# Optimization experiments

Hardware: AMD Instinct MI355X
Metric: run time of the kernel (lower is better)

Reference implementation:

```python
import jax, jax.numpy as jnp
import numpy as np

C = 256
C8 = C // 8  # query/key channels
B, T, W, H = 4, 8, 32, 32


def setup_inputs() -> dict:
    key = jax.random.key(0)
    ks = jax.random.split(key, 8)
    s = 0.05
    return {
        "x": jax.random.normal(ks[0], (B, C, T, W, H), dtype=jnp.float32),
        "wq": jax.random.normal(ks[1], (C8, C), dtype=jnp.float32) * s,
        "bq": jax.random.normal(ks[2], (C8,), dtype=jnp.float32) * s,
        "wk": jax.random.normal(ks[3], (C8, C), dtype=jnp.float32) * s,
        "bk": jax.random.normal(ks[4], (C8,), dtype=jnp.float32) * s,
        "wv": jax.random.normal(ks[5], (C, C), dtype=jnp.float32) * s,
        "bv": jax.random.normal(ks[6], (C,), dtype=jnp.float32) * s,
        "gamma": jax.random.normal(ks[7], (1,), dtype=jnp.float32),
    }


def reference(x, wq, bq, wk, bk, wv, bv, gamma):
    b, c, t, w, h = x.shape
    n = w * h
    # Faithful to torch: x.view(-1, c, w, h) is a row-major reinterpretation
    xr = jnp.reshape(x, (-1, c, n))  # (m, C, N), m = B*T
    # 1x1 convs == per-pixel linear projections
    q = jnp.einsum("oc,mcn->mno", wq, xr) + bq            # (m, N, C8)
    k = jnp.einsum("oc,mcn->mon", wk, xr) + bk[:, None]   # (m, C8, N)
    v = jnp.einsum("oc,mcn->mon", wv, xr) + bv[:, None]   # (m, C, N)
    energy = jnp.einsum("mic,mcj->mij", q, k)             # (m, N, N), unscaled
    attention = jax.nn.softmax(energy, axis=-1)
    out = jnp.einsum("mcn,mnj->mcj", v, attention)        # V @ A (as in torch code)
    out = jnp.reshape(out, (b, c, t, w, h))
    return gamma * out + x
```

## Files before the change

### kernel.cpp

```cpp
#include <hip/hip_runtime.h>

#define MB    32
#define CCH   256
#define QCH   32
#define NPIX  1024
#define SLICE (CCH * NPIX)
#define L2E   1.44269504088896340736f
#define SHIFT 32.0f

typedef __bf16          bf16x8 __attribute__((ext_vector_type(8)));
typedef __bf16          bf16x4 __attribute__((ext_vector_type(4)));
typedef float           f32x4  __attribute__((ext_vector_type(4)));
typedef unsigned int    u32x4  __attribute__((ext_vector_type(4)));
typedef unsigned short  u16x4  __attribute__((ext_vector_type(4)));

__device__ __forceinline__ unsigned short f2bf(float f) {
    unsigned int u = __builtin_bit_cast(unsigned int, f);
    u += 0x7FFFu + ((u >> 16) & 1u);
    return (unsigned short)(u >> 16);
}
__device__ __forceinline__ u16x4 cvt4(float a, float b, float c, float d) {
    bf16x4 v = { (__bf16)a, (__bf16)b, (__bf16)c, (__bf16)d };
    return __builtin_bit_cast(u16x4, v);
}
__device__ __forceinline__ float bf2f(unsigned short u) {
    unsigned int v = (unsigned int)u << 16;
    return __builtin_bit_cast(float, v);
}
__device__ __forceinline__ bf16x8 ldfrag(const unsigned short* p) {
    u32x4 u = *(const u32x4*)p;
    return __builtin_bit_cast(bf16x8, u);
}

#define WB_OFF  0u
#define QT_OFF  262144u
#define KT_OFF  2359296u
#define V_OFF   4456448u
#define A2F_OFF 21233664u

__global__ __launch_bounds__(256) void k_prep_w(
    const float* __restrict__ wq, const float* __restrict__ wk,
    const float* __restrict__ wv, unsigned short* __restrict__ Wb)
{
    int i4 = (blockIdx.x * 256 + threadIdx.x) * 4;
    int o = i4 >> 8, c = i4 & 255;
    const float* src = (o < 32) ? wq + (size_t)o * CCH + c
                     : (o < 64) ? wk + (size_t)(o - 32) * CCH + c
                                : wv + (size_t)(o - 64) * CCH + c;
    float4 v = *(const float4*)src;
    *(u16x4*)(Wb + i4) = cvt4(v.x, v.y, v.z, v.w);
}

__global__ __launch_bounds__(256) void k_proj(
    const float* __restrict__ x, const unsigned short* __restrict__ Wb,
    const float* __restrict__ bq, const float* __restrict__ bk,
    const float* __restrict__ bv,
    unsigned short* __restrict__ Qt, unsigned short* __restrict__ Kt,
    unsigned short* __restrict__ V)
{
    __shared__ unsigned short Xs[64 * 268];

    const int t = threadIdx.x, lane = t & 63, w = t >> 6;
    const int lj = lane & 15, q = lane >> 4;
    const int n0 = blockIdx.x * 64;
    const int mi = blockIdx.y;
    const float* xp = x + (size_t)mi * SLICE;

#pragma unroll
    for (int r = 0; r < 8; ++r) {
        int job = t + r * 256;
        int cp = job >> 4;
        int seg = job & 15;
        float4 va = *(const float4*)(xp + (size_t)(2 * cp) * NPIX + n0 + seg * 4);
        float4 vb = *(const float4*)(xp + (size_t)(2 * cp + 1) * NPIX + n0 + seg * 4);
        u16x4 da = cvt4(va.x, va.y, va.z, va.w);
        u16x4 db = cvt4(vb.x, vb.y, vb.z, vb.w);
#pragma unroll
        for (int e = 0; e < 4; ++e) {
            unsigned pk = (unsigned)da[e] | ((unsigned)db[e] << 16);
            *(unsigned*)&Xs[(seg * 4 + e) * 268 + 2 * cp] = pk;
        }
    }
    __syncthreads();

    f32x4 acc[5][4];
#pragma unroll
    for (int i = 0; i < 5; ++i)
#pragma unroll
        for (int b = 0; b < 4; ++b) acc[i][b] = (f32x4){0.f, 0.f, 0.f, 0.f};

    const unsigned short* wbase = Wb + (size_t)(w * 16 + lj) * CCH + q * 8;
    const unsigned short* xbase = &Xs[lj * 268 + q * 8];

#pragma unroll 2
    for (int kc = 0; kc < CCH; kc += 32) {
        bf16x8 a[5];
#pragma unroll
        for (int i = 0; i < 5; ++i)
            a[i] = ldfrag(wbase + (size_t)i * 64 * CCH + kc);
        bf16x8 xb[4];
#pragma unroll
        for (int b = 0; b < 4; ++b)
            xb[b] = ldfrag(xbase + b * 16 * 268 + kc);
#pragma unroll
        for (int i = 0; i < 5; ++i)
#pragma unroll
            for (int b = 0; b < 4; ++b)
                acc[i][b] = (i == 0)
                    ? __builtin_amdgcn_mfma_f32_16x16x32_bf16(a[i], xb[b], acc[i][b], 0, 0, 0)
                    : __builtin_amdgcn_mfma_f32_16x16x32_bf16(xb[b], a[i], acc[i][b], 0, 0, 0);
    }

#pragma unroll
    for (int i = 0; i < 5; ++i) {
        if (i == 0) {
            const int ob = w * 16 + 4 * q;
            if (w < 2) {
                unsigned short* Qp = Qt + (size_t)mi * NPIX * QCH;
                float b0 = bq[ob], b1 = bq[ob + 1], b2 = bq[ob + 2], b3 = bq[ob + 3];
#pragma unroll
                for (int b = 0; b < 4; ++b) {
                    int n = n0 + b * 16 + lj;
                    *(u16x4*)(Qp + (size_t)n * QCH + ob) =
                        cvt4((acc[i][b][0] + b0) * L2E, (acc[i][b][1] + b1) * L2E,
                             (acc[i][b][2] + b2) * L2E, (acc[i][b][3] + b3) * L2E);
                }
            } else {
                unsigned short* Kp = Kt + (size_t)mi * NPIX * QCH;
                int o2 = ob - 32;
                float b0 = bk[o2], b1 = bk[o2 + 1], b2 = bk[o2 + 2], b3 = bk[o2 + 3];
#pragma unroll
                for (int b = 0; b < 4; ++b) {
                    int n = n0 + b * 16 + lj;
                    *(u16x4*)(Kp + (size_t)n * QCH + o2) =
                        cvt4(acc[i][b][0] + b0, acc[i][b][1] + b1,
                             acc[i][b][2] + b2, acc[i][b][3] + b3);
                }
            }
        } else {
            unsigned short* Vw = V + (size_t)mi * SLICE;
            const int c16 = w + 4 * (i - 1);
            const float bb = bv[c16 * 16 + lj];
            const int n05 = n0 >> 5;
#pragma unroll
            for (int b = 0; b < 4; ++b) {
                const int l = lj | (((b & 1) * 2 + (q >> 1)) << 4);
                size_t base = ((size_t)(c16 * 32 + n05 + (b >> 1)) * 64 + l) * 8 + (q & 1) * 4;
                *(u16x4*)(Vw + base) = cvt4(acc[i][b][0] + bb, acc[i][b][1] + bb,
                                            acc[i][b][2] + bb, acc[i][b][3] + bb);
            }
        }
    }
}

__global__ __launch_bounds__(256) void k_stats(
    const unsigned short* __restrict__ Qt, const unsigned short* __restrict__ Kt,
    float* __restrict__ a2f)
{
    const int t = threadIdx.x, lane = t & 63, w = t >> 6;
    const int lj = lane & 15, q = lane >> 4;
    const int n16 = blockIdx.x * 64 + w * 16;
    const int mi = blockIdx.y;
    const unsigned short* Qp = Qt + (size_t)mi * NPIX * QCH;
    const unsigned short* Kp = Kt + (size_t)mi * NPIX * QCH;

    bf16x8 qa = ldfrag(Qp + (size_t)(n16 + lj) * QCH + q * 8);

    float s[4] = { 0.f, 0.f, 0.f, 0.f };
#pragma unroll 8
    for (int jc = 0; jc < NPIX; jc += 16) {
        bf16x8 kb = ldfrag(Kp + (size_t)(jc + lj) * QCH + q * 8);
        f32x4 z = (f32x4){0.f, 0.f, 0.f, 0.f};
        f32x4 e = __builtin_amdgcn_mfma_f32_16x16x32_bf16(qa, kb, z, 0, 0, 0);
#pragma unroll
        for (int r = 0; r < 4; ++r) s[r] += exp2f(e[r] - SHIFT);
    }
#pragma unroll
    for (int msk = 1; msk <= 8; msk <<= 1)
#pragma unroll
        for (int r = 0; r < 4; ++r) s[r] += __shfl_xor(s[r], msk, 64);
    if (lj == 0) {
        float* apo = a2f + (size_t)mi * NPIX;
#pragma unroll
        for (int r = 0; r < 4; ++r)
            apo[n16 + 4 * q + r] = SHIFT + log2f(s[r]);
    }
}

__global__ __launch_bounds__(256) void k_fused(
    const float* __restrict__ x, const float* __restrict__ gamma,
    const unsigned short* __restrict__ Qt, const unsigned short* __restrict__ Kt,
    const unsigned short* __restrict__ Vf, const float* __restrict__ a2f,
    float* __restrict__ out)
{
    __shared__ unsigned short Vs[2][8192];
    __shared__ unsigned short Ps[4][32][36];

    const int b = blockIdx.x;
    const int mi  = (b & 7) | ((b >> 7) << 3);
    const int sub = (b >> 3) & 15;
    const int j0  = (sub & 7) * 128;
    const int cb  = sub >> 3;

    const int t = threadIdx.x, lane = t & 63, w = t >> 6;
    const int lj = lane & 15, q = lane >> 4;
    const int jw = j0 + w * 32;

    const unsigned short* Qp = Qt + (size_t)mi * NPIX * QCH;
    const unsigned short* Kp = Kt + (size_t)mi * NPIX * QCH;
    const unsigned short* Vp = Vf + (size_t)mi * SLICE;
    const float* ap = a2f + (size_t)mi * NPIX;

    bf16x8 kb[2];
#pragma unroll
    for (int sj = 0; sj < 2; ++sj)
        kb[sj] = ldfrag(Kp + (size_t)(jw + sj * 16 + lj) * QCH + q * 8);

    const int fs = t >> 5, ln0 = (t & 31) * 2;
    const unsigned short* vsrc0 = Vp + ((size_t)(cb * 8 + fs) * 32) * 512 + ln0 * 8;

    f32x4 acc[8][2];
#pragma unroll
    for (int ci = 0; ci < 8; ++ci)
#pragma unroll
        for (int ji = 0; ji < 2; ++ji) acc[ci][ji] = (f32x4){0.f, 0.f, 0.f, 0.f};

    {
        u32x4 a0 = *(const u32x4*)(vsrc0);
        u32x4 a1 = *(const u32x4*)(vsrc0 + 8);
        u32x4 b0 = *(const u32x4*)(vsrc0 + 512);
        u32x4 b1 = *(const u32x4*)(vsrc0 + 520);
        *(u32x4*)&Vs[0][fs * 512 + ln0 * 8]            = a0;
        *(u32x4*)&Vs[0][fs * 512 + ln0 * 8 + 8]        = a1;
        *(u32x4*)&Vs[0][4096 + fs * 512 + ln0 * 8]     = b0;
        *(u32x4*)&Vs[0][4096 + fs * 512 + ln0 * 8 + 8] = b1;
    }
    bf16x8 qa[2][2];
    f32x4  a4[2][2];
#pragma unroll
    for (int h = 0; h < 2; ++h)
#pragma unroll
        for (int sn = 0; sn < 2; ++sn) {
            qa[h][sn] = ldfrag(Qp + (size_t)(h * 32 + sn * 16 + lj) * QCH + q * 8);
            a4[h][sn] = *(const f32x4*)(ap + h * 32 + sn * 16 + 4 * q);
        }
    __syncthreads();

    int p = 0;
    for (int nc = 0; nc < NPIX; nc += 64, p ^= 1) {
        const int n1 = (nc + 64) & (NPIX - 1);
        const unsigned short* vs = vsrc0 + (size_t)(n1 >> 5) * 512;
        u32x4 nv0 = *(const u32x4*)vs;
        u32x4 nv1 = *(const u32x4*)(vs + 8);
        u32x4 nv2 = *(const u32x4*)(vs + 512);
        u32x4 nv3 = *(const u32x4*)(vs + 520);
        bf16x8 qa_n[2][2];
        f32x4  a4_n[2][2];
#pragma unroll
        for (int h = 0; h < 2; ++h)
#pragma unroll
            for (int sn = 0; sn < 2; ++sn) {
                qa_n[h][sn] = ldfrag(Qp + (size_t)(n1 + h * 32 + sn * 16 + lj) * QCH + q * 8);
                a4_n[h][sn] = *(const f32x4*)(ap + n1 + h * 32 + sn * 16 + 4 * q);
            }

#pragma unroll
        for (int h = 0; h < 2; ++h) {
#pragma unroll
            for (int sj = 0; sj < 2; ++sj) {
                f32x4 z = (f32x4){0.f, 0.f, 0.f, 0.f};
                f32x4 e0 = __builtin_amdgcn_mfma_f32_16x16x32_bf16(qa[h][0], kb[sj], z, 0, 0, 0);
                f32x4 e1 = __builtin_amdgcn_mfma_f32_16x16x32_bf16(qa[h][1], kb[sj], z, 0, 0, 0);
                *(u16x4*)&Ps[w][sj * 16 + lj][4 * q] =
                    cvt4(exp2f(e0[0] - a4[h][0][0]), exp2f(e0[1] - a4[h][0][1]),
                         exp2f(e0[2] - a4[h][0][2]), exp2f(e0[3] - a4[h][0][3]));
                *(u16x4*)&Ps[w][sj * 16 + lj][16 + 4 * q] =
                    cvt4(exp2f(e1[0] - a4[h][1][0]), exp2f(e1[1] - a4[h][1][1]),
                         exp2f(e1[2] - a4[h][1][2]), exp2f(e1[3] - a4[h][1][3]));
            }
            bf16x8 pf[2];
#pragma unroll
            for (int ji = 0; ji < 2; ++ji)
                pf[ji] = ldfrag(&Ps[w][ji * 16 + lj][q * 8]);
            __builtin_amdgcn_s_setprio(1);
#pragma unroll
            for (int ci = 0; ci < 8; ++ci) {
                bf16x8 vfr = ldfrag(&Vs[p][h * 4096 + ci * 512 + lane * 8]);
#pragma unroll
                for (int ji = 0; ji < 2; ++ji)
                    acc[ci][ji] = __builtin_amdgcn_mfma_f32_16x16x32_bf16(vfr, pf[ji], acc[ci][ji], 0, 0, 0);
            }
            __builtin_amdgcn_s_setprio(0);
        }

        *(u32x4*)&Vs[p ^ 1][fs * 512 + ln0 * 8]            = nv0;
        *(u32x4*)&Vs[p ^ 1][fs * 512 + ln0 * 8 + 8]        = nv1;
        *(u32x4*)&Vs[p ^ 1][4096 + fs * 512 + ln0 * 8]     = nv2;
        *(u32x4*)&Vs[p ^ 1][4096 + fs * 512 + ln0 * 8 + 8] = nv3;
        __syncthreads();
#pragma unroll
        for (int h = 0; h < 2; ++h)
#pragma unroll
            for (int sn = 0; sn < 2; ++sn) { qa[h][sn] = qa_n[h][sn]; a4[h][sn] = a4_n[h][sn]; }
    }

    const float g = gamma[0];
    const size_t obase = (size_t)mi * SLICE;
#pragma unroll
    for (int ci = 0; ci < 8; ++ci) {
#pragma unroll
        for (int ji = 0; ji < 2; ++ji) {
#pragma unroll
            for (int r = 0; r < 4; ++r) {
                int c = cb * 128 + ci * 16 + 4 * q + r;
                int j = jw + ji * 16 + lj;
                size_t off = obase + (size_t)c * NPIX + j;
                out[off] = g * acc[ci][ji][r] + x[off];
            }
        }
    }
}

extern "C" void kernel_launch(void* const* d_in, const int* in_sizes, int n_in,
                              void* d_out, int out_size, void* d_ws, size_t ws_size,
                              hipStream_t stream)
{
    const float* x     = (const float*)d_in[0];
    const float* wq    = (const float*)d_in[1];
    const float* bq    = (const float*)d_in[2];
    const float* wk    = (const float*)d_in[3];
    const float* bk    = (const float*)d_in[4];
    const float* wv    = (const float*)d_in[5];
    const float* bv    = (const float*)d_in[6];
    const float* gamma = (const float*)d_in[7];
    float* out = (float*)d_out;

    char* wsb = (char*)d_ws;
    unsigned short* Wb = (unsigned short*)(wsb + WB_OFF);
    unsigned short* Qt = (unsigned short*)(wsb + QT_OFF);
    unsigned short* Kt = (unsigned short*)(wsb + KT_OFF);
    unsigned short* V  = (unsigned short*)(wsb + V_OFF);
    float*          a2 = (float*)(wsb + A2F_OFF);

    k_prep_w<<<80, 256, 0, stream>>>(wq, wk, wv, Wb);
    k_proj<<<dim3(NPIX / 64, MB), 256, 0, stream>>>(x, Wb, bq, bk, bv, Qt, Kt, V);
    k_stats<<<dim3(NPIX / 64, MB), 256, 0, stream>>>(Qt, Kt, a2);
    k_fused<<<512, 256, 0, stream>>>(x, gamma, Qt, Kt, V, a2, out);
}
```

Baseline: 169.5 us.

## Split fused attention over more channel blocks and spread stats over key ranges

The fused kernel now covers 64 channels per block instead of 128, doubling the grid to 1024 blocks. This halves the accumulator registers and the V shared-memory buffer, and adds a launch bound of 4 blocks per CU to raise occupancy. The cost is that the QK^T and exp work is recomputed twice as often, since each block redoes it for its own channel slice. The stats kernel now gives each block 16 query rows, with the four waves splitting the key range and reducing their sums through shared memory, which launches four times as many blocks.

New measurement: 188.0 us. 1.11x slower.

```diff
diff --git a/kernel.cpp b/kernel.cpp
--- a/kernel.cpp
+++ b/kernel.cpp
@@ -157,9 +157,11 @@
     const unsigned short* __restrict__ Qt, const unsigned short* __restrict__ Kt,
     float* __restrict__ a2f)
 {
+    __shared__ float sm[4][16];
+
     const int t = threadIdx.x, lane = t & 63, w = t >> 6;
     const int lj = lane & 15, q = lane >> 4;
-    const int n16 = blockIdx.x * 64 + w * 16;
+    const int n16 = blockIdx.x * 16;
     const int mi = blockIdx.y;
     const unsigned short* Qp = Qt + (size_t)mi * NPIX * QCH;
     const unsigned short* Kp = Kt + (size_t)mi * NPIX * QCH;
@@ -167,8 +169,9 @@
     bf16x8 qa = ldfrag(Qp + (size_t)(n16 + lj) * QCH + q * 8);
 
     float s[4] = { 0.f, 0.f, 0.f, 0.f };
+    const int jb = w * 256;
 #pragma unroll 8
-    for (int jc = 0; jc < NPIX; jc += 16) {
+    for (int jc = jb; jc < jb + 256; jc += 16) {
         bf16x8 kb = ldfrag(Kp + (size_t)(jc + lj) * QCH + q * 8);
         f32x4 z = (f32x4){0.f, 0.f, 0.f, 0.f};
         f32x4 e = __builtin_amdgcn_mfma_f32_16x16x32_bf16(qa, kb, z, 0, 0, 0);
@@ -180,25 +183,28 @@
 #pragma unroll
         for (int r = 0; r < 4; ++r) s[r] += __shfl_xor(s[r], msk, 64);
     if (lj == 0) {
-        float* apo = a2f + (size_t)mi * NPIX;
-#pragma unroll
-        for (int r = 0; r < 4; ++r)
-            apo[n16 + 4 * q + r] = SHIFT + log2f(s[r]);
-    }
-}
-
-__global__ __launch_bounds__(256) void k_fused(
+#pragma unroll
+        for (int r = 0; r < 4; ++r) sm[w][4 * q + r] = s[r];
+    }
+    __syncthreads();
+    if (t < 16) {
+        float S = sm[0][t] + sm[1][t] + sm[2][t] + sm[3][t];
+        a2f[(size_t)mi * NPIX + n16 + t] = SHIFT + log2f(S);
+    }
+}
+
+__global__ __launch_bounds__(256, 4) void k_fused(
     const float* __restrict__ x, const float* __restrict__ gamma,
     const unsigned short* __restrict__ Qt, const unsigned short* __restrict__ Kt,
     const unsigned short* __restrict__ Vf, const float* __restrict__ a2f,
     float* __restrict__ out)
 {
-    __shared__ unsigned short Vs[2][8192];
+    __shared__ unsigned short Vs[2][4096];
     __shared__ unsigned short Ps[4][32][36];
 
     const int b = blockIdx.x;
-    const int mi  = (b & 7) | ((b >> 7) << 3);
-    const int sub = (b >> 3) & 15;
+    const int mi  = (b & 7) | ((b >> 8) << 3);
+    const int sub = (b >> 3) & 31;
     const int j0  = (sub & 7) * 128;
     const int cb  = sub >> 3;
 
@@ -216,24 +222,22 @@
     for (int sj = 0; sj < 2; ++sj)
         kb[sj] = ldfrag(Kp + (size_t)(jw + sj * 16 + lj) * QCH + q * 8);
 
-    const int fs = t >> 5, ln0 = (t & 31) * 2;
-    const unsigned short* vsrc0 = Vp + ((size_t)(cb * 8 + fs) * 32) * 512 + ln0 * 8;
-
-    f32x4 acc[8][2];
-#pragma unroll
-    for (int ci = 0; ci < 8; ++ci)
+    const int fs = t >> 5;
+    const int ln0 = (t & 31) * 2;
+    const unsigned short* vsrc0 = Vp
+        + ((size_t)((cb * 4 + (fs & 3)) * 32) + (fs >> 2)) * 512 + ln0 * 8;
+
+    f32x4 acc[4][2];
+#pragma unroll
+    for (int ci = 0; ci < 4; ++ci)
 #pragma unroll
         for (int ji = 0; ji < 2; ++ji) acc[ci][ji] = (f32x4){0.f, 0.f, 0.f, 0.f};
 
     {
-        u32x4 a0 = *(const u32x4*)(vsrc0);
-        u32x4 a1 = *(const u32x4*)(vsrc0 + 8);
-        u32x4 b0 = *(const u32x4*)(vsrc0 + 512);
-        u32x4 b1 = *(const u32x4*)(vsrc0 + 520);
-        *(u32x4*)&Vs[0][fs * 512 + ln0 * 8]            = a0;
-        *(u32x4*)&Vs[0][fs * 512 + ln0 * 8 + 8]        = a1;
-        *(u32x4*)&Vs[0][4096 + fs * 512 + ln0 * 8]     = b0;
-        *(u32x4*)&Vs[0][4096 + fs * 512 + ln0 * 8 + 8] = b1;
+        u32x4 d0 = *(const u32x4*)vsrc0;
+        u32x4 d1 = *(const u32x4*)(vsrc0 + 8);
+        *(u32x4*)&Vs[0][fs * 512 + ln0 * 8] = d0;
+        *(u32x4*)&Vs[0][fs * 512 + ln0 * 8 + 8] = d1;
     }
     bf16x8 qa[2][2];
     f32x4  a4[2][2];
@@ -249,11 +253,9 @@
     int p = 0;
     for (int nc = 0; nc < NPIX; nc += 64, p ^= 1) {
         const int n1 = (nc + 64) & (NPIX - 1);
-        const unsigned short* vs = vsrc0 + (size_t)(n1 >> 5) * 512;
+        const unsigned short* vs = vsrc0 + (size_t)(n1 >> 6) * 1024;
         u32x4 nv0 = *(const u32x4*)vs;
         u32x4 nv1 = *(const u32x4*)(vs + 8);
-        u32x4 nv2 = *(const u32x4*)(vs + 512);
-        u32x4 nv3 = *(const u32x4*)(vs + 520);
         bf16x8 qa_n[2][2];
         f32x4  a4_n[2][2];
 #pragma unroll
@@ -284,8 +286,8 @@
                 pf[ji] = ldfrag(&Ps[w][ji * 16 + lj][q * 8]);
             __builtin_amdgcn_s_setprio(1);
 #pragma unroll
-            for (int ci = 0; ci < 8; ++ci) {
-                bf16x8 vfr = ldfrag(&Vs[p][h * 4096 + ci * 512 + lane * 8]);
+            for (int ci = 0; ci < 4; ++ci) {
+                bf16x8 vfr = ldfrag(&Vs[p][(h * 4 + ci) * 512 + lane * 8]);
 #pragma unroll
                 for (int ji = 0; ji < 2; ++ji)
                     acc[ci][ji] = __builtin_amdgcn_mfma_f32_16x16x32_bf16(vfr, pf[ji], acc[ci][ji], 0, 0, 0);
@@ -293,10 +295,8 @@
             __builtin_amdgcn_s_setprio(0);
         }
 
-        *(u32x4*)&Vs[p ^ 1][fs * 512 + ln0 * 8]            = nv0;
-        *(u32x4*)&Vs[p ^ 1][fs * 512 + ln0 * 8 + 8]        = nv1;
-        *(u32x4*)&Vs[p ^ 1][4096 + fs * 512 + ln0 * 8]     = nv2;
-        *(u32x4*)&Vs[p ^ 1][4096 + fs * 512 + ln0 * 8 + 8] = nv3;
+        *(u32x4*)&Vs[p ^ 1][fs * 512 + ln0 * 8] = nv0;
+        *(u32x4*)&Vs[p ^ 1][fs * 512 + ln0 * 8 + 8] = nv1;
         __syncthreads();
 #pragma unroll
         for (int h = 0; h < 2; ++h)
@@ -307,12 +307,12 @@
     const float g = gamma[0];
     const size_t obase = (size_t)mi * SLICE;
 #pragma unroll
-    for (int ci = 0; ci < 8; ++ci) {
+    for (int ci = 0; ci < 4; ++ci) {
 #pragma unroll
         for (int ji = 0; ji < 2; ++ji) {
 #pragma unroll
             for (int r = 0; r < 4; ++r) {
-                int c = cb * 128 + ci * 16 + 4 * q + r;
+                int c = cb * 64 + ci * 16 + 4 * q + r;
                 int j = jw + ji * 16 + lj;
                 size_t off = obase + (size_t)c * NPIX + j;
                 out[off] = g * acc[ci][ji][r] + x[off];
@@ -344,6 +344,6 @@
 
     k_prep_w<<<80, 256, 0, stream>>>(wq, wk, wv, Wb);
     k_proj<<<dim3(NPIX / 64, MB), 256, 0, stream>>>(x, Wb, bq, bk, bv, Qt, Kt, V);
-    k_stats<<<dim3(NPIX / 64, MB), 256, 0, stream>>>(Qt, Kt, a2);
-    k_fused<<<512, 256, 0, stream>>>(x, gamma, Qt, Kt, V, a2, out);
-}
+    k_stats<<<dim3(NPIX / 16, MB), 256, 0, stream>>>(Qt, Kt, a2);
+    k_fused<<<1024, 256, 0, stream>>>(x, gamma, Qt, Kt, V, a2, out);
+}
```
